# Performance work log

Hardware: AMD Instinct MI355X
Metric: run time of the kernel (lower is better)

Reference implementation:

```python
import jax, jax.numpy as jnp
import numpy as np

NUM_TOKENS = 16384
INPUT_DIM = 4096
NUM_EXPERTS = 64
TOPK = 2


def setup_inputs() -> dict:
    key = jax.random.key(0)
    k1, k2 = jax.random.split(key)
    tokens = jax.random.normal(k1, (NUM_TOKENS, INPUT_DIM), dtype=jnp.float32)
    # nn.Linear(input_dim, num_experts).weight has shape [num_experts, input_dim]
    W = jax.random.normal(k2, (NUM_EXPERTS, INPUT_DIM), dtype=jnp.float32) * (1.0 / np.sqrt(INPUT_DIM))
    return {"tokens": tokens, "W": W}


def reference(tokens, W):
    # logits: [num_tokens, num_experts] = tokens @ W.T
    logits = jnp.einsum("td,ed->te", tokens, W)
    scores = jax.nn.softmax(logits, axis=-1)
    topk_scores, topk_indices = jax.lax.top_k(scores, TOPK)
    return topk_scores, topk_indices
```

## Files before the change

kernel.cpp:

```cpp
#include <hip/hip_runtime.h>
#include <math.h>

#define NTOK 16384
#define DIM  4096
#define NEXP 64
#define KS   4
#define KSL  (DIM / KS)
#define NCH  (KSL / 32)
#define BM   64

typedef __fp16 f16x8 __attribute__((ext_vector_type(8)));
typedef __fp16 f16x2 __attribute__((ext_vector_type(2)));
typedef float  f32x4 __attribute__((ext_vector_type(4)));

__device__ __forceinline__ void gl_lds16(const void* g, void* l) {
  __builtin_amdgcn_global_load_lds(
      (const __attribute__((address_space(1))) void*)g,
      (__attribute__((address_space(3))) void*)l, 16, 0, 0);
}

__global__ __launch_bounds__(256) void split_w(
    const float* __restrict__ W,
    __fp16* __restrict__ Wh,
    __fp16* __restrict__ Wl)
{
  const int i = blockIdx.x * 256 + threadIdx.x;
  const float w = W[i];
  const __fp16 h = (__fp16)w;
  const float r = w - (float)h;
  Wh[i] = h;
  Wl[i] = (__fp16)r;
}

__global__ __launch_bounds__(256, 4) void router_mfma(
    const float* __restrict__ tokens,
    const __fp16* __restrict__ Wh,
    const __fp16* __restrict__ Wl,
    float* __restrict__ partial)
{
  __shared__ float  As[2][BM * 32];
  __shared__ __fp16 Bh[2][NEXP * 32];
  __shared__ __fp16 Bl[2][NEXP * 32];

  const int tid  = threadIdx.x;
  const int wid  = tid >> 6;
  const int lane = tid & 63;
  const int rc   = lane & 15;
  const int q    = lane >> 4;
  const int s    = blockIdx.x & (KS - 1);
  const int rowbase = (blockIdx.x >> 2) * BM;
  const int wrow    = rowbase + 16 * wid;
  const int kbase   = s * KSL;

  const int a_tl = lane >> 3, a_j = lane & 7;
  const float* asrc0 = tokens + (size_t)(wrow + a_tl) * DIM + kbase
                       + ((a_j ^ a_tl) << 2);
  const float* asrc1 = asrc0 + (size_t)8 * DIM;
  const int b_el = lane >> 2, b_j = lane & 3;
  const size_t boff = (size_t)(16 * wid + b_el) * DIM + kbase
                      + ((b_j ^ (b_el & 3)) << 3);
  const __fp16* bsrc_h = Wh + boff;
  const __fp16* bsrc_l = Wl + boff;

#define STAGE(buf, c) {                                        \
    const int ko = (c) * 32;                                   \
    gl_lds16(asrc0 + ko,  &As[buf][(16 * wid) * 32]);          \
    gl_lds16(asrc1 + ko,  &As[buf][(16 * wid + 8) * 32]);      \
    gl_lds16(bsrc_h + ko, &Bh[buf][(16 * wid) * 32]);          \
    gl_lds16(bsrc_l + ko, &Bl[buf][(16 * wid) * 32]);          \
  }

  f32x4 acc0 = {0.f,0.f,0.f,0.f}, acc1 = {0.f,0.f,0.f,0.f};
  f32x4 acc2 = {0.f,0.f,0.f,0.f}, acc3 = {0.f,0.f,0.f,0.f};

  const int sa0 = (2 * q) ^ (rc & 7), sa1 = (2 * q + 1) ^ (rc & 7);
  const int sb  = q ^ (rc & 3);
  const int arow = (16 * wid + rc) * 32;

#define COMP(buf) {                                                          \
    const float4 a0 = *(const float4*)(&As[buf][arow + sa0 * 4]);            \
    const float4 a1 = *(const float4*)(&As[buf][arow + sa1 * 4]);            \
    const f16x8 bh0 = *(const f16x8*)(&Bh[buf][( 0 + rc) * 32 + sb * 8]);    \
    const f16x8 bh1 = *(const f16x8*)(&Bh[buf][(16 + rc) * 32 + sb * 8]);    \
    const f16x8 bh2 = *(const f16x8*)(&Bh[buf][(32 + rc) * 32 + sb * 8]);    \
    const f16x8 bh3 = *(const f16x8*)(&Bh[buf][(48 + rc) * 32 + sb * 8]);    \
    const f16x8 bl0 = *(const f16x8*)(&Bl[buf][( 0 + rc) * 32 + sb * 8]);    \
    const f16x8 bl1 = *(const f16x8*)(&Bl[buf][(16 + rc) * 32 + sb * 8]);    \
    const f16x8 bl2 = *(const f16x8*)(&Bl[buf][(32 + rc) * 32 + sb * 8]);    \
    const f16x8 bl3 = *(const f16x8*)(&Bl[buf][(48 + rc) * 32 + sb * 8]);    \
    const f16x2 h0 = __builtin_amdgcn_cvt_pkrtz(a0.x, a0.y);                 \
    const f16x2 h1 = __builtin_amdgcn_cvt_pkrtz(a0.z, a0.w);                 \
    const f16x2 h2 = __builtin_amdgcn_cvt_pkrtz(a1.x, a1.y);                 \
    const f16x2 h3 = __builtin_amdgcn_cvt_pkrtz(a1.z, a1.w);                 \
    const f16x2 m0 = __builtin_amdgcn_cvt_pkrtz(a0.x - (float)h0[0],         \
                                                a0.y - (float)h0[1]);        \
    const f16x2 m1 = __builtin_amdgcn_cvt_pkrtz(a0.z - (float)h1[0],         \
                                                a0.w - (float)h1[1]);        \
    const f16x2 m2 = __builtin_amdgcn_cvt_pkrtz(a1.x - (float)h2[0],         \
                                                a1.y - (float)h2[1]);        \
    const f16x2 m3 = __builtin_amdgcn_cvt_pkrtz(a1.z - (float)h3[0],         \
                                                a1.w - (float)h3[1]);        \
    const f16x8 Ah = {h0[0],h0[1],h1[0],h1[1],h2[0],h2[1],h3[0],h3[1]};      \
    const f16x8 Am = {m0[0],m0[1],m1[0],m1[1],m2[0],m2[1],m3[0],m3[1]};      \
    acc0 = __builtin_amdgcn_mfma_f32_16x16x32_f16(Ah, bh0, acc0, 0, 0, 0);   \
    acc1 = __builtin_amdgcn_mfma_f32_16x16x32_f16(Ah, bh1, acc1, 0, 0, 0);   \
    acc2 = __builtin_amdgcn_mfma_f32_16x16x32_f16(Ah, bh2, acc2, 0, 0, 0);   \
    acc3 = __builtin_amdgcn_mfma_f32_16x16x32_f16(Ah, bh3, acc3, 0, 0, 0);   \
    acc0 = __builtin_amdgcn_mfma_f32_16x16x32_f16(Ah, bl0, acc0, 0, 0, 0);   \
    acc1 = __builtin_amdgcn_mfma_f32_16x16x32_f16(Ah, bl1, acc1, 0, 0, 0);   \
    acc2 = __builtin_amdgcn_mfma_f32_16x16x32_f16(Ah, bl2, acc2, 0, 0, 0);   \
    acc3 = __builtin_amdgcn_mfma_f32_16x16x32_f16(Ah, bl3, acc3, 0, 0, 0);   \
    acc0 = __builtin_amdgcn_mfma_f32_16x16x32_f16(Am, bh0, acc0, 0, 0, 0);   \
    acc1 = __builtin_amdgcn_mfma_f32_16x16x32_f16(Am, bh1, acc1, 0, 0, 0);   \
    acc2 = __builtin_amdgcn_mfma_f32_16x16x32_f16(Am, bh2, acc2, 0, 0, 0);   \
    acc3 = __builtin_amdgcn_mfma_f32_16x16x32_f16(Am, bh3, acc3, 0, 0, 0);   \
  }

  STAGE(0, 0);
  __syncthreads();

  for (int c = 0; c < NCH; c += 2) {
    if (c + 1 < NCH) STAGE(1, c + 1);
    COMP(0);
    __syncthreads();
    if (c + 2 < NCH) STAGE(0, c + 2);
    COMP(1);
    __syncthreads();
  }
#undef STAGE
#undef COMP

  float* P = partial + ((size_t)s * NTOK + wrow) * NEXP;
  #pragma unroll
  for (int rr = 0; rr < 4; ++rr) {
    const int row = q * 4 + rr;
    P[(size_t)row * NEXP +  0 + rc] = acc0[rr];
    P[(size_t)row * NEXP + 16 + rc] = acc1[rr];
    P[(size_t)row * NEXP + 32 + rc] = acc2[rr];
    P[(size_t)row * NEXP + 48 + rc] = acc3[rr];
  }
}

__global__ __launch_bounds__(64) void router_finish(
    const float* __restrict__ partial,
    float* __restrict__ out)
{
  const int t = blockIdx.x * 64 + threadIdx.x;

  float l[NEXP];
  const float* p0 = partial + (size_t)t * NEXP;
  #pragma unroll
  for (int qq = 0; qq < 16; ++qq) {
    const float4 v = *(const float4*)(p0 + qq * 4);
    l[qq*4+0] = v.x; l[qq*4+1] = v.y; l[qq*4+2] = v.z; l[qq*4+3] = v.w;
  }
  #pragma unroll
  for (int s = 1; s < KS; ++s) {
    const float* p = partial + ((size_t)s * NTOK + t) * NEXP;
    #pragma unroll
    for (int qq = 0; qq < 16; ++qq) {
      const float4 v = *(const float4*)(p + qq * 4);
      l[qq*4+0] += v.x; l[qq*4+1] += v.y; l[qq*4+2] += v.z; l[qq*4+3] += v.w;
    }
  }

  float t1v = l[0]; int t1i = 0;
  float t2v = -INFINITY; int t2i = NEXP;
  #pragma unroll
  for (int e = 1; e < NEXP; ++e) {
    const float v = l[e];
    if (v > t1v) { t2v = t1v; t2i = t1i; t1v = v; t1i = e; }
    else if (v > t2v) { t2v = v; t2i = e; }
  }

  float ssum = 0.f;
  #pragma unroll
  for (int e = 0; e < NEXP; ++e) ssum += expf(l[e] - t1v);

  const float inv = 1.0f / ssum;
  out[t * 2 + 0] = inv;
  out[t * 2 + 1] = expf(t2v - t1v) * inv;
  out[2 * NTOK + t * 2 + 0] = (float)t1i;
  out[2 * NTOK + t * 2 + 1] = (float)t2i;
}

extern "C" void kernel_launch(void* const* d_in, const int* in_sizes, int n_in,
                              void* d_out, int out_size, void* d_ws, size_t ws_size,
                              hipStream_t stream) {
  const float* tokens = (const float*)d_in[0];
  const float* W      = (const float*)d_in[1];
  float* out          = (float*)d_out;

  __fp16* Wh = (__fp16*)d_ws;
  __fp16* Wl = Wh + (size_t)NEXP * DIM;
  float* partial = (float*)((char*)d_ws + (size_t)2 * NEXP * DIM * sizeof(__fp16));

  split_w<<<(NEXP * DIM) / 256, 256, 0, stream>>>(W, Wh, Wl);
  router_mfma<<<(NTOK / BM) * KS, 256, 0, stream>>>(tokens, Wh, Wl, partial);
  router_finish<<<NTOK / 64, 64, 0, stream>>>(partial, out);
}
```

Baseline: 78.68 us.

## Load W directly to registers and use per-wave triple-buffered token staging without barriers

The W half/low fragments are now read straight from global memory (L2/L1-cached) into registers instead of being staged through shared memory. Each wave stages only its own 16 token rows into a private triple-buffered LDS region. Waits use explicit vmcnt counters instead of block-wide __syncthreads, which removes block synchronisation and shrinks LDS use. The cost is more global load traffic for W per wave, and correctness now depends on hand-tuned vmcnt values matching the issue order of loads.

```diff
diff --git a/kernel.cpp b/kernel.cpp
--- a/kernel.cpp
+++ b/kernel.cpp
@@ -38,9 +38,7 @@
     const __fp16* __restrict__ Wl,
     float* __restrict__ partial)
 {
-  __shared__ float  As[2][BM * 32];
-  __shared__ __fp16 Bh[2][NEXP * 32];
-  __shared__ __fp16 Bl[2][NEXP * 32];
+  __shared__ float As[4][3][16 * 32];
 
   const int tid  = threadIdx.x;
   const int wid  = tid >> 6;
@@ -48,46 +46,42 @@
   const int rc   = lane & 15;
   const int q    = lane >> 4;
   const int s    = blockIdx.x & (KS - 1);
-  const int rowbase = (blockIdx.x >> 2) * BM;
-  const int wrow    = rowbase + 16 * wid;
-  const int kbase   = s * KSL;
+  const int wrow = (blockIdx.x >> 2) * BM + 16 * wid;
+  const int kbase = s * KSL;
 
   const int a_tl = lane >> 3, a_j = lane & 7;
   const float* asrc0 = tokens + (size_t)(wrow + a_tl) * DIM + kbase
                        + ((a_j ^ a_tl) << 2);
   const float* asrc1 = asrc0 + (size_t)8 * DIM;
-  const int b_el = lane >> 2, b_j = lane & 3;
-  const size_t boff = (size_t)(16 * wid + b_el) * DIM + kbase
-                      + ((b_j ^ (b_el & 3)) << 3);
-  const __fp16* bsrc_h = Wh + boff;
-  const __fp16* bsrc_l = Wl + boff;
 
-#define STAGE(buf, c) {                                        \
-    const int ko = (c) * 32;                                   \
-    gl_lds16(asrc0 + ko,  &As[buf][(16 * wid) * 32]);          \
-    gl_lds16(asrc1 + ko,  &As[buf][(16 * wid + 8) * 32]);      \
-    gl_lds16(bsrc_h + ko, &Bh[buf][(16 * wid) * 32]);          \
-    gl_lds16(bsrc_l + ko, &Bl[buf][(16 * wid) * 32]);          \
+  const f16x8* bp0 = (const f16x8*)(Wh + (size_t)( 0 + rc) * DIM + kbase + q * 8);
+  const f16x8* bp1 = (const f16x8*)(Wh + (size_t)(16 + rc) * DIM + kbase + q * 8);
+  const f16x8* bp2 = (const f16x8*)(Wh + (size_t)(32 + rc) * DIM + kbase + q * 8);
+  const f16x8* bp3 = (const f16x8*)(Wh + (size_t)(48 + rc) * DIM + kbase + q * 8);
+  const f16x8* lp0 = (const f16x8*)(Wl + (size_t)( 0 + rc) * DIM + kbase + q * 8);
+  const f16x8* lp1 = (const f16x8*)(Wl + (size_t)(16 + rc) * DIM + kbase + q * 8);
+  const f16x8* lp2 = (const f16x8*)(Wl + (size_t)(32 + rc) * DIM + kbase + q * 8);
+  const f16x8* lp3 = (const f16x8*)(Wl + (size_t)(48 + rc) * DIM + kbase + q * 8);
+
+  f32x4 acc0 = {0,0,0,0}, acc1 = {0,0,0,0}, acc2 = {0,0,0,0}, acc3 = {0,0,0,0};
+
+  const int sa0 = (2 * q) ^ (rc & 7), sa1 = (2 * q + 1) ^ (rc & 7);
+
+#define STAGE(buf, c) {                               \
+    const int ko = (c) * 32;                          \
+    gl_lds16(asrc0 + ko, &As[wid][buf][0]);           \
+    gl_lds16(asrc1 + ko, &As[wid][buf][8 * 32]);      \
   }
 
-  f32x4 acc0 = {0.f,0.f,0.f,0.f}, acc1 = {0.f,0.f,0.f,0.f};
-  f32x4 acc2 = {0.f,0.f,0.f,0.f}, acc3 = {0.f,0.f,0.f,0.f};
+#define VM(n) asm volatile("s_waitcnt vmcnt(" #n ")" ::: "memory")
 
-  const int sa0 = (2 * q) ^ (rc & 7), sa1 = (2 * q + 1) ^ (rc & 7);
-  const int sb  = q ^ (rc & 3);
-  const int arow = (16 * wid + rc) * 32;
-
-#define COMP(buf) {                                                          \
-    const float4 a0 = *(const float4*)(&As[buf][arow + sa0 * 4]);            \
-    const float4 a1 = *(const float4*)(&As[buf][arow + sa1 * 4]);            \
-    const f16x8 bh0 = *(const f16x8*)(&Bh[buf][( 0 + rc) * 32 + sb * 8]);    \
-    const f16x8 bh1 = *(const f16x8*)(&Bh[buf][(16 + rc) * 32 + sb * 8]);    \
-    const f16x8 bh2 = *(const f16x8*)(&Bh[buf][(32 + rc) * 32 + sb * 8]);    \
-    const f16x8 bh3 = *(const f16x8*)(&Bh[buf][(48 + rc) * 32 + sb * 8]);    \
-    const f16x8 bl0 = *(const f16x8*)(&Bl[buf][( 0 + rc) * 32 + sb * 8]);    \
-    const f16x8 bl1 = *(const f16x8*)(&Bl[buf][(16 + rc) * 32 + sb * 8]);    \
-    const f16x8 bl2 = *(const f16x8*)(&Bl[buf][(32 + rc) * 32 + sb * 8]);    \
-    const f16x8 bl3 = *(const f16x8*)(&Bl[buf][(48 + rc) * 32 + sb * 8]);    \
+#define COMP(buf, c) {                                                       \
+    const float4 a0 = *(const float4*)(&As[wid][buf][rc * 32 + sa0 * 4]);    \
+    const float4 a1 = *(const float4*)(&As[wid][buf][rc * 32 + sa1 * 4]);    \
+    const f16x8 bh0 = bp0[4 * (c)]; const f16x8 bh1 = bp1[4 * (c)];          \
+    const f16x8 bh2 = bp2[4 * (c)]; const f16x8 bh3 = bp3[4 * (c)];          \
+    const f16x8 bl0 = lp0[4 * (c)]; const f16x8 bl1 = lp1[4 * (c)];          \
+    const f16x8 bl2 = lp2[4 * (c)]; const f16x8 bl3 = lp3[4 * (c)];          \
     const f16x2 h0 = __builtin_amdgcn_cvt_pkrtz(a0.x, a0.y);                 \
     const f16x2 h1 = __builtin_amdgcn_cvt_pkrtz(a0.z, a0.w);                 \
     const f16x2 h2 = __builtin_amdgcn_cvt_pkrtz(a1.x, a1.y);                 \
@@ -106,29 +100,31 @@
     acc1 = __builtin_amdgcn_mfma_f32_16x16x32_f16(Ah, bh1, acc1, 0, 0, 0);   \
     acc2 = __builtin_amdgcn_mfma_f32_16x16x32_f16(Ah, bh2, acc2, 0, 0, 0);   \
     acc3 = __builtin_amdgcn_mfma_f32_16x16x32_f16(Ah, bh3, acc3, 0, 0, 0);   \
+    acc0 = __builtin_amdgcn_mfma_f32_16x16x32_f16(Am, bh0, acc0, 0, 0, 0);   \
+    acc1 = __builtin_amdgcn_mfma_f32_16x16x32_f16(Am, bh1, acc1, 0, 0, 0);   \
+    acc2 = __builtin_amdgcn_mfma_f32_16x16x32_f16(Am, bh2, acc2, 0, 0, 0);   \
+    acc3 = __builtin_amdgcn_mfma_f32_16x16x32_f16(Am, bh3, acc3, 0, 0, 0);   \
     acc0 = __builtin_amdgcn_mfma_f32_16x16x32_f16(Ah, bl0, acc0, 0, 0, 0);   \
     acc1 = __builtin_amdgcn_mfma_f32_16x16x32_f16(Ah, bl1, acc1, 0, 0, 0);   \
     acc2 = __builtin_amdgcn_mfma_f32_16x16x32_f16(Ah, bl2, acc2, 0, 0, 0);   \
     acc3 = __builtin_amdgcn_mfma_f32_16x16x32_f16(Ah, bl3, acc3, 0, 0, 0);   \
-    acc0 = __builtin_amdgcn_mfma_f32_16x16x32_f16(Am, bh0, acc0, 0, 0, 0);   \
-    acc1 = __builtin_amdgcn_mfma_f32_16x16x32_f16(Am, bh1, acc1, 0, 0, 0);   \
-    acc2 = __builtin_amdgcn_mfma_f32_16x16x32_f16(Am, bh2, acc2, 0, 0, 0);   \
-    acc3 = __builtin_amdgcn_mfma_f32_16x16x32_f16(Am, bh3, acc3, 0, 0, 0);   \
   }
 
-  STAGE(0, 0);
-  __syncthreads();
-
-  for (int c = 0; c < NCH; c += 2) {
-    if (c + 1 < NCH) STAGE(1, c + 1);
-    COMP(0);
-    __syncthreads();
-    if (c + 2 < NCH) STAGE(0, c + 2);
-    COMP(1);
-    __syncthreads();
+  STAGE(0, 0); STAGE(1, 1);
+  STAGE(2, 2); VM(4);  COMP(0, 0);
+  for (int i = 0; i < 9; ++i) {
+    const int c = 1 + 3 * i;
+    STAGE(0, c + 2); VM(12); COMP(1, c);
+    STAGE(1, c + 3); VM(12); COMP(2, c + 1);
+    STAGE(2, c + 4); VM(12); COMP(0, c + 2);
   }
+  STAGE(0, 30); VM(12); COMP(1, 28);
+  STAGE(1, 31); VM(12); COMP(2, 29);
+  VM(2);  COMP(0, 30);
+  VM(0);  COMP(1, 31);
 #undef STAGE
 #undef COMP
+#undef VM
 
   float* P = partial + ((size_t)s * NTOK + wrow) * NEXP;
   #pragma unroll
```

New measurement: 163.3 us. 2.08x slower.

## Switch router GEMM to 32x32x16 MFMA with 2x2 wave tiling and BK=64

Applied to the files above, without the earlier changes.

Replaces the per-wave 16-row by 64-expert tiling built from 16x16x32 MFMAs with a 2x2 wave grid where each wave computes a 32x32 tile using 32x32x16 MFMAs. The K chunk grows from 32 to 64 and the split-K factor drops from 4 to 2, so there are fewer partial sums to write and reduce and fewer barriers per unit of work. The aim is to cut LDS B-operand reads and the cost of converting A to fp16, since each wave now converts only its own 32 rows once per K step. The trade-off is a larger LDS footprint and an occupancy hint lowered from 4 to 2 blocks per CU, and half as many blocks, which could reduce latency hiding.

```diff
diff --git a/kernel.cpp b/kernel.cpp
--- a/kernel.cpp
+++ b/kernel.cpp
@@ -4,14 +4,15 @@
 #define NTOK 16384
 #define DIM  4096
 #define NEXP 64
-#define KS   4
+#define KS   2
 #define KSL  (DIM / KS)
-#define NCH  (KSL / 32)
+#define BK   64
+#define NCH  (KSL / BK)
 #define BM   64
 
-typedef __fp16 f16x8 __attribute__((ext_vector_type(8)));
-typedef __fp16 f16x2 __attribute__((ext_vector_type(2)));
-typedef float  f32x4 __attribute__((ext_vector_type(4)));
+typedef __fp16 f16x8  __attribute__((ext_vector_type(8)));
+typedef __fp16 f16x2  __attribute__((ext_vector_type(2)));
+typedef float  f32x16 __attribute__((ext_vector_type(16)));
 
 __device__ __forceinline__ void gl_lds16(const void* g, void* l) {
   __builtin_amdgcn_global_load_lds(
@@ -32,62 +33,66 @@
   Wl[i] = (__fp16)r;
 }
 
-__global__ __launch_bounds__(256, 4) void router_mfma(
+__global__ __launch_bounds__(256, 2) void router_mfma(
     const float* __restrict__ tokens,
     const __fp16* __restrict__ Wh,
     const __fp16* __restrict__ Wl,
     float* __restrict__ partial)
 {
-  __shared__ float  As[2][BM * 32];
-  __shared__ __fp16 Bh[2][NEXP * 32];
-  __shared__ __fp16 Bl[2][NEXP * 32];
+  __shared__ float  As[2][BM * BK];
+  __shared__ __fp16 Bh[2][NEXP * BK];
+  __shared__ __fp16 Bl[2][NEXP * BK];
 
   const int tid  = threadIdx.x;
   const int wid  = tid >> 6;
   const int lane = tid & 63;
-  const int rc   = lane & 15;
-  const int q    = lane >> 4;
+  const int rc2  = lane & 31;
+  const int q2   = lane >> 5;
+  const int wr   = wid >> 1;
+  const int ec   = wid & 1;
   const int s    = blockIdx.x & (KS - 1);
-  const int rowbase = (blockIdx.x >> 2) * BM;
-  const int wrow    = rowbase + 16 * wid;
-  const int kbase   = s * KSL;
+  const int tb   = (blockIdx.x >> 1) * BM;
+  const int kbase = s * KSL;
 
-  const int a_tl = lane >> 3, a_j = lane & 7;
-  const float* asrc0 = tokens + (size_t)(wrow + a_tl) * DIM + kbase
-                       + ((a_j ^ a_tl) << 2);
-  const float* asrc1 = asrc0 + (size_t)8 * DIM;
-  const int b_el = lane >> 2, b_j = lane & 3;
-  const size_t boff = (size_t)(16 * wid + b_el) * DIM + kbase
-                      + ((b_j ^ (b_el & 3)) << 3);
-  const __fp16* bsrc_h = Wh + boff;
-  const __fp16* bsrc_l = Wl + boff;
+  const int l16 = lane >> 4;
+  const int aj  = lane & 15;
+  const float* ap0 = tokens + (size_t)(tb + 16*wid +  0 + l16) * DIM + kbase + ((aj ^ ( 0 + l16)) << 2);
+  const float* ap1 = tokens + (size_t)(tb + 16*wid +  4 + l16) * DIM + kbase + ((aj ^ ( 4 + l16)) << 2);
+  const float* ap2 = tokens + (size_t)(tb + 16*wid +  8 + l16) * DIM + kbase + ((aj ^ ( 8 + l16)) << 2);
+  const float* ap3 = tokens + (size_t)(tb + 16*wid + 12 + l16) * DIM + kbase + ((aj ^ (12 + l16)) << 2);
+  const int l8 = lane >> 3;
+  const int bj = lane & 7;
+  const size_t bo0 = (size_t)(16*wid + 0 + l8) * DIM + kbase + ((bj ^ l8) << 3);
+  const size_t bo1 = (size_t)(16*wid + 8 + l8) * DIM + kbase + ((bj ^ l8) << 3);
+  const __fp16* bh0s = Wh + bo0; const __fp16* bh1s = Wh + bo1;
+  const __fp16* bl0s = Wl + bo0; const __fp16* bl1s = Wl + bo1;
 
-#define STAGE(buf, c) {                                        \
-    const int ko = (c) * 32;                                   \
-    gl_lds16(asrc0 + ko,  &As[buf][(16 * wid) * 32]);          \
-    gl_lds16(asrc1 + ko,  &As[buf][(16 * wid + 8) * 32]);      \
-    gl_lds16(bsrc_h + ko, &Bh[buf][(16 * wid) * 32]);          \
-    gl_lds16(bsrc_l + ko, &Bl[buf][(16 * wid) * 32]);          \
+#define STAGE(buf, c) {                                          \
+    const int ko = (c) * BK;                                     \
+    gl_lds16(ap0 + ko, &As[buf][(16 * wid +  0) * BK]);          \
+    gl_lds16(ap1 + ko, &As[buf][(16 * wid +  4) * BK]);          \
+    gl_lds16(ap2 + ko, &As[buf][(16 * wid +  8) * BK]);          \
+    gl_lds16(ap3 + ko, &As[buf][(16 * wid + 12) * BK]);          \
+    gl_lds16(bh0s + ko, &Bh[buf][(16 * wid + 0) * BK]);          \
+    gl_lds16(bh1s + ko, &Bh[buf][(16 * wid + 8) * BK]);          \
+    gl_lds16(bl0s + ko, &Bl[buf][(16 * wid + 0) * BK]);          \
+    gl_lds16(bl1s + ko, &Bl[buf][(16 * wid + 8) * BK]);          \
   }
 
-  f32x4 acc0 = {0.f,0.f,0.f,0.f}, acc1 = {0.f,0.f,0.f,0.f};
-  f32x4 acc2 = {0.f,0.f,0.f,0.f}, acc3 = {0.f,0.f,0.f,0.f};
+  f32x16 acc = {0,0,0,0, 0,0,0,0, 0,0,0,0, 0,0,0,0};
 
-  const int sa0 = (2 * q) ^ (rc & 7), sa1 = (2 * q + 1) ^ (rc & 7);
-  const int sb  = q ^ (rc & 3);
-  const int arow = (16 * wid + rc) * 32;
+  const int akey = rc2 & 15;
+  const int bkey = rc2 & 7;
+  const int Arow = (32 * wr + rc2) * BK;
+  const int Brow = (32 * ec + rc2) * BK;
 
-#define COMP(buf) {                                                          \
-    const float4 a0 = *(const float4*)(&As[buf][arow + sa0 * 4]);            \
-    const float4 a1 = *(const float4*)(&As[buf][arow + sa1 * 4]);            \
-    const f16x8 bh0 = *(const f16x8*)(&Bh[buf][( 0 + rc) * 32 + sb * 8]);    \
-    const f16x8 bh1 = *(const f16x8*)(&Bh[buf][(16 + rc) * 32 + sb * 8]);    \
-    const f16x8 bh2 = *(const f16x8*)(&Bh[buf][(32 + rc) * 32 + sb * 8]);    \
-    const f16x8 bh3 = *(const f16x8*)(&Bh[buf][(48 + rc) * 32 + sb * 8]);    \
-    const f16x8 bl0 = *(const f16x8*)(&Bl[buf][( 0 + rc) * 32 + sb * 8]);    \
-    const f16x8 bl1 = *(const f16x8*)(&Bl[buf][(16 + rc) * 32 + sb * 8]);    \
-    const f16x8 bl2 = *(const f16x8*)(&Bl[buf][(32 + rc) * 32 + sb * 8]);    \
-    const f16x8 bl3 = *(const f16x8*)(&Bl[buf][(48 + rc) * 32 + sb * 8]);    \
+#define KSTEP(buf, kk) {                                                     \
+    const int u0 = 4 * (kk) + 2 * q2;                                        \
+    const float4 a0 = *(const float4*)(&As[buf][Arow + ((u0    ) ^ akey) * 4]); \
+    const float4 a1 = *(const float4*)(&As[buf][Arow + ((u0 + 1) ^ akey) * 4]); \
+    const int ub = ((2 * (kk) + q2) ^ bkey) * 8;                             \
+    const f16x8 bhv = *(const f16x8*)(&Bh[buf][Brow + ub]);                  \
+    const f16x8 blv = *(const f16x8*)(&Bl[buf][Brow + ub]);                  \
     const f16x2 h0 = __builtin_amdgcn_cvt_pkrtz(a0.x, a0.y);                 \
     const f16x2 h1 = __builtin_amdgcn_cvt_pkrtz(a0.z, a0.w);                 \
     const f16x2 h2 = __builtin_amdgcn_cvt_pkrtz(a1.x, a1.y);                 \
@@ -102,19 +107,12 @@
                                                 a1.w - (float)h3[1]);        \
     const f16x8 Ah = {h0[0],h0[1],h1[0],h1[1],h2[0],h2[1],h3[0],h3[1]};      \
     const f16x8 Am = {m0[0],m0[1],m1[0],m1[1],m2[0],m2[1],m3[0],m3[1]};      \
-    acc0 = __builtin_amdgcn_mfma_f32_16x16x32_f16(Ah, bh0, acc0, 0, 0, 0);   \
-    acc1 = __builtin_amdgcn_mfma_f32_16x16x32_f16(Ah, bh1, acc1, 0, 0, 0);   \
-    acc2 = __builtin_amdgcn_mfma_f32_16x16x32_f16(Ah, bh2, acc2, 0, 0, 0);   \
-    acc3 = __builtin_amdgcn_mfma_f32_16x16x32_f16(Ah, bh3, acc3, 0, 0, 0);   \
-    acc0 = __builtin_amdgcn_mfma_f32_16x16x32_f16(Ah, bl0, acc0, 0, 0, 0);   \
-    acc1 = __builtin_amdgcn_mfma_f32_16x16x32_f16(Ah, bl1, acc1, 0, 0, 0);   \
-    acc2 = __builtin_amdgcn_mfma_f32_16x16x32_f16(Ah, bl2, acc2, 0, 0, 0);   \
-    acc3 = __builtin_amdgcn_mfma_f32_16x16x32_f16(Ah, bl3, acc3, 0, 0, 0);   \
-    acc0 = __builtin_amdgcn_mfma_f32_16x16x32_f16(Am, bh0, acc0, 0, 0, 0);   \
-    acc1 = __builtin_amdgcn_mfma_f32_16x16x32_f16(Am, bh1, acc1, 0, 0, 0);   \
-    acc2 = __builtin_amdgcn_mfma_f32_16x16x32_f16(Am, bh2, acc2, 0, 0, 0);   \
-    acc3 = __builtin_amdgcn_mfma_f32_16x16x32_f16(Am, bh3, acc3, 0, 0, 0);   \
+    acc = __builtin_amdgcn_mfma_f32_32x32x16_f16(Ah, bhv, acc, 0, 0, 0);     \
+    acc = __builtin_amdgcn_mfma_f32_32x32x16_f16(Ah, blv, acc, 0, 0, 0);     \
+    acc = __builtin_amdgcn_mfma_f32_32x32x16_f16(Am, bhv, acc, 0, 0, 0);     \
   }
+
+#define COMP(buf) { KSTEP(buf, 0); KSTEP(buf, 1); KSTEP(buf, 2); KSTEP(buf, 3); }
 
   STAGE(0, 0);
   __syncthreads();
@@ -129,15 +127,13 @@
   }
 #undef STAGE
 #undef COMP
+#undef KSTEP
 
-  float* P = partial + ((size_t)s * NTOK + wrow) * NEXP;
+  float* P = partial + ((size_t)s * NTOK + tb + 32 * wr) * NEXP + 32 * ec;
   #pragma unroll
-  for (int rr = 0; rr < 4; ++rr) {
-    const int row = q * 4 + rr;
-    P[(size_t)row * NEXP +  0 + rc] = acc0[rr];
-    P[(size_t)row * NEXP + 16 + rc] = acc1[rr];
-    P[(size_t)row * NEXP + 32 + rc] = acc2[rr];
-    P[(size_t)row * NEXP + 48 + rc] = acc3[rr];
+  for (int reg = 0; reg < 16; ++reg) {
+    const int row = (reg & 3) + 8 * (reg >> 2) + 4 * q2;
+    P[(size_t)row * NEXP + rc2] = acc[reg];
   }
 }
 
```

New measurement: 72.56 us. 7.8% less time.
